# Optimization experiments

Hardware: AMD Instinct MI355X
Metric: run time of the kernel (lower is better)

Reference implementation:

```python
import jax, jax.numpy as jnp
import numpy as np
import math

D, H, FF = 1024, 16, 4096
B, L = 4, 1024

def setup_inputs() -> dict:
    key = jax.random.key(0)
    ks = jax.random.split(key, 20)
    g = lambda k, shp: jax.random.normal(k, shp, dtype=jnp.float32) * 0.02
    inp = {
        'x': jax.random.normal(ks[0], (B, L, D), dtype=jnp.float32),
        'encoder_output': jax.random.normal(ks[1], (B, L, D), dtype=jnp.float32),
        'src_mask': jnp.ones((1, 1, L, L), dtype=jnp.int32),
        'tgt_mask': jnp.tril(jnp.ones((L, L), dtype=jnp.int32))[None, None],
        'wq': g(ks[2], (D, D)), 'bq': jnp.zeros((D,), jnp.float32),
        'wk': g(ks[3], (D, D)), 'bk': jnp.zeros((D,), jnp.float32),
        'wv': g(ks[4], (D, D)), 'bv': jnp.zeros((D,), jnp.float32),
        'wo': g(ks[5], (D, D)), 'bo': jnp.zeros((D,), jnp.float32),
        'w1': g(ks[6], (FF, D)), 'b1': jnp.zeros((FF,), jnp.float32),
        'w2': g(ks[7], (D, FF)), 'b2': jnp.zeros((D,), jnp.float32),
        'g1': jnp.ones((D,), jnp.float32), 'be1': jnp.zeros((D,), jnp.float32),
        'g2': jnp.ones((D,), jnp.float32), 'be2': jnp.zeros((D,), jnp.float32),
    }
    return inp

def _layernorm(x, g, b, eps=1e-5):
    mu = jnp.mean(x, axis=-1, keepdims=True)
    var = jnp.var(x, axis=-1, keepdims=True)
    return (x - mu) * jax.lax.rsqrt(var + eps) * g + b

def _mha(q, k, v, mask, wq, bq, wk, bk, wv, bv, wo, bo):
    Bq, Lq, C = q.shape
    dh = C // H
    qh = (q @ wq.T + bq).reshape(Bq, Lq, H, dh)      # b q h d
    kh = (k @ wk.T + bk).reshape(Bq, -1, H, dh)       # b k h d
    vh = (v @ wv.T + bv).reshape(Bq, -1, H, dh)
    # NOTE: source scales by sqrt(C) (full model dim), not sqrt(head_dim)
    scores = jnp.einsum('bqhd,bkhd->bhqk', qh, kh) / math.sqrt(C)
    if mask is not None:
        scores = jnp.where(mask == 0, jnp.float32(-1e9), scores)
    attn = jax.nn.softmax(scores, axis=-1)
    out = jnp.einsum('bhqk,bkhd->bqhd', attn, vh).reshape(Bq, Lq, C)
    return out @ wo.T + bo

def reference(x, encoder_output, src_mask, tgt_mask,
              wq, bq, wk, bk, wv, bv, wo, bo,
              w1, b1, w2, b2, g1, be1, g2, be2):
    # self-attention (dropout identity in eval mode)
    y1 = _mha(x, x, x, tgt_mask, wq, bq, wk, bk, wv, bv, wo, bo)
    y1 = _layernorm(y1 + x, g1, be1)
    # cross-attention: source reuses attn1 weights and layer_norm1 (faithful)
    y2 = _mha(y1, encoder_output, encoder_output, src_mask, wq, bq, wk, bk, wv, bv, wo, bo)
    y2 = _layernorm(y1 + y2, g1, be1)
    # FFN + layer_norm2
    y = jax.nn.relu(y2 @ w1.T + b1) @ w2.T + b2
    return _layernorm(y2 + y, g2, be2)
```

## Files before the change

### kernel.cpp

```cpp
#include <hip/hip_runtime.h>
#include <hip/hip_bf16.h>

typedef __attribute__((ext_vector_type(8))) short short8;
typedef __attribute__((ext_vector_type(4))) float f32x4;
typedef __attribute__((ext_vector_type(4))) unsigned short ushort4v;

#define MFMA_BF16(a, b, c) __builtin_amdgcn_mfma_f32_16x16x32_bf16((a), (b), (c), 0, 0, 0)
#define AS1 __attribute__((address_space(1)))
#define AS3 __attribute__((address_space(3)))

__device__ __forceinline__ unsigned short f2b(float f) {
  unsigned u = __float_as_uint(f);
  u += 0x7fffu + ((u >> 16) & 1u);
  return (unsigned short)(u >> 16);
}

__device__ __forceinline__ size_t kpack_idx(int row, int col) {
  int b = row >> 10, l = row & 1023, h = col >> 6, d = col & 63;
  return ((size_t)(b * 16 + h) << 16) + l * 64 + (d ^ ((l & 7) << 3));
}

__global__ __launch_bounds__(256) void cast8(
    const float* s0, const float* s1, const float* s2, const float* s3,
    const float* s4, const float* s5, const float* s6, const float* s7,
    unsigned short* d0, unsigned short* d1, unsigned short* d2, unsigned short* d3,
    unsigned short* d4, unsigned short* d5, unsigned short* d6, unsigned short* d7,
    int n0, int n1, int n2, int n3, int n4, int n5, int n6, int n7) {
  const float* s; unsigned short* d; int n;
  switch (blockIdx.y) {
    case 0: s = s0; d = d0; n = n0; break;
    case 1: s = s1; d = d1; n = n1; break;
    case 2: s = s2; d = d2; n = n2; break;
    case 3: s = s3; d = d3; n = n3; break;
    case 4: s = s4; d = d4; n = n4; break;
    case 5: s = s5; d = d5; n = n5; break;
    case 6: s = s6; d = d6; n = n6; break;
    default: s = s7; d = d7; n = n7; break;
  }
  int stride = gridDim.x * blockDim.x;
  for (int i = blockIdx.x * blockDim.x + threadIdx.x; i < n; i += stride) {
    float4 v = reinterpret_cast<const float4*>(s)[i];
    ushort4v o;
    o.x = f2b(v.x); o.y = f2b(v.y); o.z = f2b(v.z); o.w = f2b(v.w);
    reinterpret_cast<ushort4v*>(d)[i] = o;
  }
}

template <int RELU, int RES, int OUTF, int OUTB, int TM>
__global__ __launch_bounds__(256) void gemm_bt(
    const unsigned short* __restrict__ A, const unsigned short* __restrict__ W,
    const float* __restrict__ bias, const float* __restrict__ resid,
    float* __restrict__ outF, unsigned short* __restrict__ outB,
    int M, int N, int K) {
  constexpr int MI = TM / 32;
  __shared__ unsigned short lA[TM * 64];
  __shared__ unsigned short lB[128 * 64];
  int nbn = N >> 7;
  int nwg = gridDim.x;
  int id = blockIdx.x;
  { int q = nwg >> 3; id = (id & 7) * q + (id >> 3); }
  int m0 = (id / nbn) * TM, n0 = (id % nbn) << 7;
  int lane = threadIdx.x & 63, wave = threadIdx.x >> 6;
  int wr = (wave >> 1) * (TM / 2), wc = (wave & 1) * 64;
  int rq = lane & 15, kq = (lane >> 4) * 8;
  int xr8 = (rq & 7) << 3;
  f32x4 acc[MI][4] = {};

  int t8 = threadIdx.x * 8;
  for (int kt = 0; kt < K; kt += 64) {
#pragma unroll
    for (int i = 0; i < MI; ++i) {
      int e = t8 + i * 2048;
      int row = e >> 6;
      int gcol = (((e >> 3) & 7) ^ (row & 7)) << 3;
      __builtin_amdgcn_global_load_lds(
          (const AS1 void*)(A + (size_t)(m0 + row) * K + kt + gcol),
          (AS3 void*)(lA + e), 16, 0, 0);
    }
#pragma unroll
    for (int i = 0; i < 4; ++i) {
      int e = t8 + i * 2048;
      int row = e >> 6;
      int gcol = (((e >> 3) & 7) ^ (row & 7)) << 3;
      __builtin_amdgcn_global_load_lds(
          (const AS1 void*)(W + (size_t)(n0 + row) * K + kt + gcol),
          (AS3 void*)(lB + e), 16, 0, 0);
    }
    __syncthreads();
#pragma unroll
    for (int s = 0; s < 2; ++s) {
      short8 af[MI], bf[4];
#pragma unroll
      for (int i = 0; i < MI; ++i)
        af[i] = *reinterpret_cast<const short8*>(lA + (wr + i * 16 + rq) * 64 + ((s * 32 + kq) ^ xr8));
#pragma unroll
      for (int j = 0; j < 4; ++j)
        bf[j] = *reinterpret_cast<const short8*>(lB + (wc + j * 16 + rq) * 64 + ((s * 32 + kq) ^ xr8));
#pragma unroll
      for (int i = 0; i < MI; ++i)
#pragma unroll
        for (int j = 0; j < 4; ++j)
          acc[i][j] = MFMA_BF16(af[i], bf[j], acc[i][j]);
    }
    __syncthreads();
  }

  int r0 = (lane >> 4) * 4;
#pragma unroll
  for (int i = 0; i < MI; ++i) {
#pragma unroll
    for (int j = 0; j < 4; ++j) {
      int row = m0 + wr + i * 16 + r0;
      int col = n0 + wc + j * 16 + rq;
      float bv = bias[col];
#pragma unroll
      for (int r = 0; r < 4; ++r) {
        float v = acc[i][j][r] + bv;
        if (RES) v += resid[(size_t)(row + r) * N + col];
        if (RELU) v = fmaxf(v, 0.0f);
        if (OUTF) outF[(size_t)(row + r) * N + col] = v;
        if (OUTB) outB[(size_t)(row + r) * N + col] = f2b(v);
      }
    }
  }
}

__global__ __launch_bounds__(256, 2) void gemm_qkv_f(
    const unsigned short* __restrict__ xb, const unsigned short* __restrict__ encb,
    const unsigned short* __restrict__ wq, const unsigned short* __restrict__ wk,
    const unsigned short* __restrict__ wv,
    const float* __restrict__ bq, const float* __restrict__ bk, const float* __restrict__ bv,
    unsigned short* __restrict__ qb, unsigned short* __restrict__ kp1,
    unsigned short* __restrict__ vp1, unsigned short* __restrict__ kp2,
    unsigned short* __restrict__ vp2) {
  __shared__ unsigned short lA[2][4096];
  __shared__ unsigned short lB[2][3][4096];
  int id = blockIdx.x;
  id = (id & 7) * 64 + (id >> 3);
  int sel = id >> 8;
  int idx = id & 255;
  int m0 = (idx >> 3) << 7, col0 = (idx & 7) << 7;
  int nW = sel ? 2 : 3;
  const unsigned short* A = sel ? encb : xb;
  const unsigned short* W0 = sel ? wk : wq;
  const unsigned short* W1 = sel ? wv : wk;
  const unsigned short* W2 = wv;
  int lane = threadIdx.x & 63, wave = threadIdx.x >> 6;
  int wr = (wave >> 1) * 64, wc = (wave & 1) * 64;
  int rq = lane & 15, kq = (lane >> 4) * 8;
  f32x4 acc[3][4][4] = {};

  int e0 = threadIdx.x * 8;
#define STG(KT, BUF)                                                            \
  {                                                                             \
    _Pragma("unroll") for (int i = 0; i < 2; ++i) {                             \
      int e = e0 + i * 2048;                                                    \
      int row = e >> 5, col = e & 31;                                           \
      __builtin_amdgcn_global_load_lds(                                         \
          (const AS1 void*)(A + (size_t)(m0 + row) * 1024 + (KT) + col),        \
          (AS3 void*)(&lA[BUF][e]), 16, 0, 0);                                  \
      __builtin_amdgcn_global_load_lds(                                         \
          (const AS1 void*)(W0 + (size_t)(col0 + row) * 1024 + (KT) + col),     \
          (AS3 void*)(&lB[BUF][0][e]), 16, 0, 0);                               \
      __builtin_amdgcn_global_load_lds(                                         \
          (const AS1 void*)(W1 + (size_t)(col0 + row) * 1024 + (KT) + col),     \
          (AS3 void*)(&lB[BUF][1][e]), 16, 0, 0);                               \
      if (!sel)                                                                 \
        __builtin_amdgcn_global_load_lds(                                       \
            (const AS1 void*)(W2 + (size_t)(col0 + row) * 1024 + (KT) + col),   \
            (AS3 void*)(&lB[BUF][2][e]), 16, 0, 0);                             \
    }                                                                           \
  }

  STG(0, 0);
  __syncthreads();
  for (int t = 0; t < 32; ++t) {
    int cur = t & 1;
    if (t + 1 < 32) STG((t + 1) << 5, cur ^ 1);
    short8 af[4];
#pragma unroll
    for (int i = 0; i < 4; ++i)
      af[i] = *reinterpret_cast<const short8*>(&lA[cur][(wr + i * 16 + rq) * 32 + kq]);
#pragma unroll
    for (int w = 0; w < 3; ++w) {
      if (w < nW) {
        short8 bf[4];
#pragma unroll
        for (int j = 0; j < 4; ++j)
          bf[j] = *reinterpret_cast<const short8*>(&lB[cur][w][(wc + j * 16 + rq) * 32 + kq]);
#pragma unroll
        for (int i = 0; i < 4; ++i)
#pragma unroll
          for (int j = 0; j < 4; ++j)
            acc[w][i][j] = MFMA_BF16(af[i], bf[j], acc[w][i][j]);
      }
    }
    __syncthreads();
  }
#undef STG

  int r0 = (lane >> 4) * 4;
#pragma unroll
  for (int w = 0; w < 3; ++w) {
    if (w >= nW) continue;
    const float* bias = sel ? (w == 0 ? bk : bv) : (w == 0 ? bq : (w == 1 ? bk : bv));
    unsigned short* outp = sel ? (w == 0 ? kp2 : vp2) : (w == 0 ? qb : (w == 1 ? kp1 : vp1));
    int pack = sel ? (w + 1) : w;
#pragma unroll
    for (int i = 0; i < 4; ++i) {
#pragma unroll
      for (int j = 0; j < 4; ++j) {
        int row0 = m0 + wr + i * 16 + r0;
        int col = col0 + wc + j * 16 + rq;
        float bv2 = bias[col];
        if (pack == 2) {
          int b = row0 >> 10, k0 = row0 & 1023, h = col >> 6, d = col & 63;
          size_t idx2 = ((size_t)((b * 16 + h) * 16 + (k0 >> 6)) << 12) + d * 64 + ((k0 & 63) ^ ((d & 7) << 3));
          ushort4v o;
          o.x = f2b(acc[w][i][j][0] + bv2);
          o.y = f2b(acc[w][i][j][1] + bv2);
          o.z = f2b(acc[w][i][j][2] + bv2);
          o.w = f2b(acc[w][i][j][3] + bv2);
          *reinterpret_cast<ushort4v*>(&outp[idx2]) = o;
        } else {
#pragma unroll
          for (int r = 0; r < 4; ++r) {
            int row = row0 + r;
            float v = acc[w][i][j][r] + bv2;
            if (pack == 0) outp[(size_t)row * 1024 + col] = f2b(v);
            else outp[kpack_idx(row, col)] = f2b(v);
          }
        }
      }
    }
  }
}

__device__ __forceinline__ void attn_step(
    const unsigned short* __restrict__ kcur, const unsigned short* __restrict__ vcur,
    unsigned short* __restrict__ plw, const short8* qf,
    f32x4* accd, float& m2, float& lsum,
    int rq, int hi, int kq, int xr, int wave, bool domask) {
  const float SC = 0.04508422f;
  f32x4 st[4];
  __builtin_amdgcn_s_setprio(1);
#pragma unroll
  for (int sub = 0; sub < 4; ++sub) {
    f32x4 z = {0.f, 0.f, 0.f, 0.f};
#pragma unroll
    for (int c = 0; c < 2; ++c) {
      short8 kf = *reinterpret_cast<const short8*>(
          &kcur[(sub * 16 + rq) * 64 + ((c * 32 + hi * 8) ^ xr)]);
      z = MFMA_BF16(kf, qf[c], z);
    }
    st[sub] = z * SC;
  }
  __builtin_amdgcn_s_setprio(0);
  if (domask) {
#pragma unroll
    for (int sub = 0; sub < 4; ++sub)
#pragma unroll
      for (int r = 0; r < 4; ++r)
        if (sub * 16 + hi * 4 + r > wave * 16 + rq) st[sub][r] = -1e9f;
  }
  f32x4 t0 = {fmaxf(st[0][0], st[1][0]), fmaxf(st[0][1], st[1][1]),
              fmaxf(st[0][2], st[1][2]), fmaxf(st[0][3], st[1][3])};
  f32x4 t1 = {fmaxf(st[2][0], st[3][0]), fmaxf(st[2][1], st[3][1]),
              fmaxf(st[2][2], st[3][2]), fmaxf(st[2][3], st[3][3])};
  float mx = fmaxf(fmaxf(fmaxf(t0[0], t1[0]), fmaxf(t0[1], t1[1])),
                   fmaxf(fmaxf(t0[2], t1[2]), fmaxf(t0[3], t1[3])));
  mx = fmaxf(mx, __shfl_xor(mx, 16, 64));
  mx = fmaxf(mx, __shfl_xor(mx, 32, 64));
  float mn = fmaxf(m2, mx);
  float al = exp2f(m2 - mn);
  m2 = mn;
  f32x4 e[4];
#pragma unroll
  for (int sub = 0; sub < 4; ++sub)
#pragma unroll
    for (int r = 0; r < 4; ++r) e[sub][r] = exp2f(st[sub][r] - mn);
  f32x4 s01 = e[0] + e[1], s23 = e[2] + e[3];
  f32x4 s = s01 + s23;
  float ps = (s[0] + s[1]) + (s[2] + s[3]);
  ps += __shfl_xor(ps, 16, 64);
  ps += __shfl_xor(ps, 32, 64);
  lsum = lsum * al + ps;
#pragma unroll
  for (int sub = 0; sub < 4; ++sub) {
    unsigned w0 = (unsigned)f2b(e[sub][0]) | ((unsigned)f2b(e[sub][1]) << 16);
    unsigned w1 = (unsigned)f2b(e[sub][2]) | ((unsigned)f2b(e[sub][3]) << 16);
    uint2 w = make_uint2(w0, w1);
    *reinterpret_cast<uint2*>(&plw[rq * 64 + ((sub * 16 + hi * 4) ^ xr)]) = w;
  }
  float alb[4];
#pragma unroll
  for (int r = 0; r < 4; ++r) alb[r] = __shfl(al, hi * 4 + r, 64);
#pragma unroll
  for (int d = 0; d < 4; ++d)
#pragma unroll
    for (int r = 0; r < 4; ++r) accd[d][r] *= alb[r];
  short8 pf[2];
#pragma unroll
  for (int c = 0; c < 2; ++c)
    pf[c] = *reinterpret_cast<const short8*>(&plw[rq * 64 + ((c * 32 + hi * 8) ^ xr)]);
  __builtin_amdgcn_s_setprio(1);
#pragma unroll
  for (int d = 0; d < 4; ++d) {
#pragma unroll
    for (int c = 0; c < 2; ++c) {
      short8 vf = *reinterpret_cast<const short8*>(
          &vcur[(d * 16 + rq) * 64 + ((c * 32 + hi * 8) ^ xr)]);
      accd[d] = MFMA_BF16(pf[c], vf, accd[d]);
    }
  }
  __builtin_amdgcn_s_setprio(0);
}

__global__ __launch_bounds__(256) void attn_kernel(
    const unsigned short* __restrict__ Q, const unsigned short* __restrict__ Kp,
    const unsigned short* __restrict__ Vp, unsigned short* __restrict__ O, int causal) {
  __shared__ unsigned short kls[2][4096];
  __shared__ unsigned short vls[2][4096];
  __shared__ unsigned short pls[4][1024];
  int id = blockIdx.x;
  int xcd = id & 7, j = id >> 3;
  int bh = xcd * 8 + (j & 7);
  int b = bh >> 4, h = bh & 15;
  int lane = threadIdx.x & 63, wave = threadIdx.x >> 6;
  int rq = lane & 15, hi = lane >> 4, kq = hi * 8;
  int xr = (rq & 7) << 3;
  int sb = wave * 1024 + lane * 8;
  const unsigned short* Kbh = Kp + ((size_t)bh << 16);
  const unsigned short* Vbh = Vp + ((size_t)bh << 16);
  unsigned short* plw = pls[wave];

  int p = j >> 3;
  int qtA = p;
  int qtB = causal ? (15 - p) : (p + 8);
  int lastA = causal ? qtA : 15;
  int nkt = causal ? (qtB + 1) : 16;

  int qrowA = qtA * 64 + wave * 16, qrowB = qtB * 64 + wave * 16;
  short8 qfA[2], qfB[2];
#pragma unroll
  for (int c = 0; c < 2; ++c) {
    qfA[c] = *reinterpret_cast<const short8*>(
        Q + (size_t)(b * 1024 + qrowA + rq) * 1024 + h * 64 + c * 32 + kq);
    qfB[c] = *reinterpret_cast<const short8*>(
        Q + (size_t)(b * 1024 + qrowB + rq) * 1024 + h * 64 + c * 32 + kq);
  }

  float mA = -1e30f, lsA = 0.f, mB = -1e30f, lsB = 0.f;
  f32x4 accA[4] = {}, accB[4] = {};

#pragma unroll
  for (int i = 0; i < 2; ++i) {
    __builtin_amdgcn_global_load_lds((const AS1 void*)(Kbh + sb + i * 512),
                                     (AS3 void*)(&kls[0][sb + i * 512]), 16, 0, 0);
    __builtin_amdgcn_global_load_lds((const AS1 void*)(Vbh + sb + i * 512),
                                     (AS3 void*)(&vls[0][sb + i * 512]), 16, 0, 0);
  }
  __syncthreads();

  int cur = 0;
  for (int kt = 0; kt < nkt; ++kt) {
    if (kt + 1 < nkt) {
      const unsigned short* kg = Kbh + (kt + 1) * 4096 + sb;
      const unsigned short* vg = Vbh + (kt + 1) * 4096 + sb;
#pragma unroll
      for (int i = 0; i < 2; ++i) {
        __builtin_amdgcn_global_load_lds((const AS1 void*)(kg + i * 512),
                                         (AS3 void*)(&kls[cur ^ 1][sb + i * 512]), 16, 0, 0);
        __builtin_amdgcn_global_load_lds((const AS1 void*)(vg + i * 512),
                                         (AS3 void*)(&vls[cur ^ 1][sb + i * 512]), 16, 0, 0);
      }
    }
    attn_step(kls[cur], vls[cur], plw, qfB, accB, mB, lsB, rq, hi, kq, xr, wave,
              causal && kt == qtB);
    if (kt <= lastA)
      attn_step(kls[cur], vls[cur], plw, qfA, accA, mA, lsA, rq, hi, kq, xr, wave,
                causal && kt == qtA);
    __syncthreads();
    cur ^= 1;
  }

  float lbA[4], lbB[4];
#pragma unroll
  for (int r = 0; r < 4; ++r) {
    lbA[r] = 1.0f / __shfl(lsA, hi * 4 + r, 64);
    lbB[r] = 1.0f / __shfl(lsB, hi * 4 + r, 64);
  }
#pragma unroll
  for (int d = 0; d < 4; ++d)
#pragma unroll
    for (int r = 0; r < 4; ++r) {
      O[(size_t)(b * 1024 + qrowA + hi * 4 + r) * 1024 + h * 64 + d * 16 + rq] =
          f2b(accA[d][r] * lbA[r]);
      O[(size_t)(b * 1024 + qrowB + hi * 4 + r) * 1024 + h * 64 + d * 16 + rq] =
          f2b(accB[d][r] * lbB[r]);
    }
}

template <int OUTF, int OUTB>
__global__ __launch_bounds__(256) void ln_kernel(const float* __restrict__ X,
                                                 const float* __restrict__ g,
                                                 const float* __restrict__ be,
                                                 float* __restrict__ outF,
                                                 unsigned short* __restrict__ outB) {
  __shared__ float red[2][4];
  int row = blockIdx.x;
  int t = threadIdx.x;
  const float* xr = X + (size_t)row * 1024;
  float4 v = reinterpret_cast<const float4*>(xr)[t];
  float s = v.x + v.y + v.z + v.w;
  float ss = v.x * v.x + v.y * v.y + v.z * v.z + v.w * v.w;
#pragma unroll
  for (int off = 1; off < 64; off <<= 1) {
    s += __shfl_xor(s, off, 64);
    ss += __shfl_xor(ss, off, 64);
  }
  int wave = t >> 6;
  if ((t & 63) == 0) { red[0][wave] = s; red[1][wave] = ss; }
  __syncthreads();
  s = red[0][0] + red[0][1] + red[0][2] + red[0][3];
  ss = red[1][0] + red[1][1] + red[1][2] + red[1][3];
  float mu = s * (1.f / 1024.f);
  float var = ss * (1.f / 1024.f) - mu * mu;
  float rs = rsqrtf(var + 1e-5f);
  float4 gv = reinterpret_cast<const float4*>(g)[t];
  float4 bv = reinterpret_cast<const float4*>(be)[t];
  float o0 = (v.x - mu) * rs * gv.x + bv.x;
  float o1 = (v.y - mu) * rs * gv.y + bv.y;
  float o2 = (v.z - mu) * rs * gv.z + bv.z;
  float o3 = (v.w - mu) * rs * gv.w + bv.w;
  if (OUTF) {
    float4 o = make_float4(o0, o1, o2, o3);
    reinterpret_cast<float4*>(outF + (size_t)row * 1024)[t] = o;
  }
  if (OUTB) {
    ushort4v o;
    o.x = f2b(o0); o.y = f2b(o1); o.z = f2b(o2); o.w = f2b(o3);
    reinterpret_cast<ushort4v*>(outB + (size_t)row * 1024)[t] = o;
  }
}

extern "C" void kernel_launch(void* const* d_in, const int* in_sizes, int n_in,
                              void* d_out, int out_size, void* d_ws, size_t ws_size,
                              hipStream_t stream) {
  const float* x   = (const float*)d_in[0];
  const float* enc = (const float*)d_in[1];
  const float* wq = (const float*)d_in[4];  const float* bq = (const float*)d_in[5];
  const float* wk = (const float*)d_in[6];  const float* bk = (const float*)d_in[7];
  const float* wv = (const float*)d_in[8];  const float* bv = (const float*)d_in[9];
  const float* wo = (const float*)d_in[10]; const float* bo = (const float*)d_in[11];
  const float* w1 = (const float*)d_in[12]; const float* b1 = (const float*)d_in[13];
  const float* w2 = (const float*)d_in[14]; const float* b2 = (const float*)d_in[15];
  const float* g1 = (const float*)d_in[16]; const float* be1 = (const float*)d_in[17];
  const float* g2 = (const float*)d_in[18]; const float* be2 = (const float*)d_in[19];
  float* out = (float*)d_out;

  const int M = 4096;
  char* ws = (char*)d_ws;
  size_t off = 0;
  auto alloc = [&](size_t bytes) -> char* {
    char* p = ws + off;
    off += (bytes + 255) & ~(size_t)255;
    return p;
  };
  unsigned short* xb   = (unsigned short*)alloc((size_t)M * 1024 * 2);
  unsigned short* encb = (unsigned short*)alloc((size_t)M * 1024 * 2);
  unsigned short* wqb  = (unsigned short*)alloc((size_t)1024 * 1024 * 2);
  unsigned short* wkb  = (unsigned short*)alloc((size_t)1024 * 1024 * 2);
  unsigned short* wvb  = (unsigned short*)alloc((size_t)1024 * 1024 * 2);
  unsigned short* wob  = (unsigned short*)alloc((size_t)1024 * 1024 * 2);
  unsigned short* w1b  = (unsigned short*)alloc((size_t)4096 * 1024 * 2);
  unsigned short* w2b  = (unsigned short*)alloc((size_t)4096 * 1024 * 2);
  unsigned short* qb   = (unsigned short*)alloc((size_t)M * 1024 * 2);
  unsigned short* kp1  = (unsigned short*)alloc((size_t)M * 1024 * 2);
  unsigned short* vp1  = (unsigned short*)alloc((size_t)M * 1024 * 2);
  unsigned short* kp2  = (unsigned short*)alloc((size_t)M * 1024 * 2);
  unsigned short* vp2  = (unsigned short*)alloc((size_t)M * 1024 * 2);
  unsigned short* ab   = (unsigned short*)alloc((size_t)M * 1024 * 2);
  float* s1 = (float*)alloc((size_t)M * 1024 * 4);
  float* y1 = (float*)alloc((size_t)M * 1024 * 4);
  unsigned short* hb = kp1;
  unsigned short* y1b = xb;
  unsigned short* y2b = qb;
  float* y2 = y1;

  dim3 b256(256);
  cast8<<<dim3(256, 8), b256, 0, stream>>>(
      x, enc, wq, wk, wv, wo, w1, w2,
      xb, encb, wqb, wkb, wvb, wob, w1b, w2b,
      M * 1024 / 4, M * 1024 / 4, 262144, 262144, 262144, 262144,
      4096 * 1024 / 4, 4096 * 1024 / 4);

  gemm_qkv_f<<<512, b256, 0, stream>>>(xb, encb, wqb, wkb, wvb, bq, bk, bv,
                                       qb, kp1, vp1, kp2, vp2);

  attn_kernel<<<512, b256, 0, stream>>>(qb, kp1, vp1, ab, 1);
  gemm_bt<0, 1, 1, 0, 64><<<512, b256, 0, stream>>>(ab, wob, bo, x, s1, nullptr, M, 1024, 1024);
  ln_kernel<1, 1><<<4096, b256, 0, stream>>>(s1, g1, be1, y1, y1b);

  gemm_bt<0, 0, 0, 1, 64><<<512, b256, 0, stream>>>(y1b, wqb, bq, nullptr, nullptr, qb, M, 1024, 1024);
  attn_kernel<<<512, b256, 0, stream>>>(qb, kp2, vp2, ab, 0);
  gemm_bt<0, 1, 1, 0, 64><<<512, b256, 0, stream>>>(ab, wob, bo, y1, s1, nullptr, M, 1024, 1024);
  ln_kernel<1, 1><<<4096, b256, 0, stream>>>(s1, g1, be1, y2, y2b);

  gemm_bt<1, 0, 0, 1, 128><<<1024, b256, 0, stream>>>(y2b, w1b, b1, nullptr, nullptr, hb, M, 4096, 1024);
  gemm_bt<0, 1, 1, 0, 64><<<512, b256, 0, stream>>>(hb, w2b, b2, y2, s1, nullptr, M, 1024, 4096);
  ln_kernel<1, 0><<<4096, b256, 0, stream>>>(s1, g2, be2, out, nullptr);

  (void)in_sizes; (void)n_in; (void)out_size; (void)ws_size;
}
```

Baseline: 341.5 us.

## Swizzle QKV GEMM LDS, add lazy softmax rescale, one q-tile per attention block

The QKV GEMM now XOR-swizzles the 16-byte column chunks it loads into LDS, and its fragment reads use the matching swizzle, to avoid LDS bank conflicts. The attention softmax skips rescaling the accumulator and running sum when no row's max grows by more than a threshold (a lazy-rescale trick), which saves exp and multiply work. The attention kernel also stops pairing two query tiles per block and launches twice as many blocks, one q-tile each, with causal tiles ordered heaviest first. The trade-off is less K/V reuse per block and more total K/V loads, in exchange for simpler blocks and better load balance.

```diff
diff --git a/kernel.cpp b/kernel.cpp
--- a/kernel.cpp
+++ b/kernel.cpp
@@ -148,6 +148,7 @@
   int lane = threadIdx.x & 63, wave = threadIdx.x >> 6;
   int wr = (wave >> 1) * 64, wc = (wave & 1) * 64;
   int rq = lane & 15, kq = (lane >> 4) * 8;
+  int xk = ((rq >> 1) & 3) << 3;
   f32x4 acc[3][4][4] = {};
 
   int e0 = threadIdx.x * 8;
@@ -155,19 +156,20 @@
   {                                                                             \
     _Pragma("unroll") for (int i = 0; i < 2; ++i) {                             \
       int e = e0 + i * 2048;                                                    \
-      int row = e >> 5, col = e & 31;                                           \
+      int row = e >> 5;                                                         \
+      int gcol = ((((e >> 3) & 3) ^ ((row >> 1) & 3)) << 3);                    \
       __builtin_amdgcn_global_load_lds(                                         \
-          (const AS1 void*)(A + (size_t)(m0 + row) * 1024 + (KT) + col),        \
+          (const AS1 void*)(A + (size_t)(m0 + row) * 1024 + (KT) + gcol),       \
           (AS3 void*)(&lA[BUF][e]), 16, 0, 0);                                  \
       __builtin_amdgcn_global_load_lds(                                         \
-          (const AS1 void*)(W0 + (size_t)(col0 + row) * 1024 + (KT) + col),     \
+          (const AS1 void*)(W0 + (size_t)(col0 + row) * 1024 + (KT) + gcol),    \
           (AS3 void*)(&lB[BUF][0][e]), 16, 0, 0);                               \
       __builtin_amdgcn_global_load_lds(                                         \
-          (const AS1 void*)(W1 + (size_t)(col0 + row) * 1024 + (KT) + col),     \
+          (const AS1 void*)(W1 + (size_t)(col0 + row) * 1024 + (KT) + gcol),    \
           (AS3 void*)(&lB[BUF][1][e]), 16, 0, 0);                               \
       if (!sel)                                                                 \
         __builtin_amdgcn_global_load_lds(                                       \
-            (const AS1 void*)(W2 + (size_t)(col0 + row) * 1024 + (KT) + col),   \
+            (const AS1 void*)(W2 + (size_t)(col0 + row) * 1024 + (KT) + gcol),  \
             (AS3 void*)(&lB[BUF][2][e]), 16, 0, 0);                             \
     }                                                                           \
   }
@@ -180,14 +182,14 @@
     short8 af[4];
 #pragma unroll
     for (int i = 0; i < 4; ++i)
-      af[i] = *reinterpret_cast<const short8*>(&lA[cur][(wr + i * 16 + rq) * 32 + kq]);
+      af[i] = *reinterpret_cast<const short8*>(&lA[cur][(wr + i * 16 + rq) * 32 + (kq ^ xk)]);
 #pragma unroll
     for (int w = 0; w < 3; ++w) {
       if (w < nW) {
         short8 bf[4];
 #pragma unroll
         for (int j = 0; j < 4; ++j)
-          bf[j] = *reinterpret_cast<const short8*>(&lB[cur][w][(wc + j * 16 + rq) * 32 + kq]);
+          bf[j] = *reinterpret_cast<const short8*>(&lB[cur][w][(wc + j * 16 + rq) * 32 + (kq ^ xk)]);
 #pragma unroll
         for (int i = 0; i < 4; ++i)
 #pragma unroll
@@ -271,9 +273,13 @@
                    fmaxf(fmaxf(t0[2], t1[2]), fmaxf(t0[3], t1[3])));
   mx = fmaxf(mx, __shfl_xor(mx, 16, 64));
   mx = fmaxf(mx, __shfl_xor(mx, 32, 64));
-  float mn = fmaxf(m2, mx);
-  float al = exp2f(m2 - mn);
-  m2 = mn;
+  int skip = __all(mx <= m2 + 4.0f);
+  float mn = m2, al = 1.0f;
+  if (!skip) {
+    mn = fmaxf(m2, mx);
+    al = exp2f(m2 - mn);
+    m2 = mn;
+  }
   f32x4 e[4];
 #pragma unroll
   for (int sub = 0; sub < 4; ++sub)
@@ -284,7 +290,6 @@
   float ps = (s[0] + s[1]) + (s[2] + s[3]);
   ps += __shfl_xor(ps, 16, 64);
   ps += __shfl_xor(ps, 32, 64);
-  lsum = lsum * al + ps;
 #pragma unroll
   for (int sub = 0; sub < 4; ++sub) {
     unsigned w0 = (unsigned)f2b(e[sub][0]) | ((unsigned)f2b(e[sub][1]) << 16);
@@ -292,13 +297,18 @@
     uint2 w = make_uint2(w0, w1);
     *reinterpret_cast<uint2*>(&plw[rq * 64 + ((sub * 16 + hi * 4) ^ xr)]) = w;
   }
-  float alb[4];
-#pragma unroll
-  for (int r = 0; r < 4; ++r) alb[r] = __shfl(al, hi * 4 + r, 64);
-#pragma unroll
-  for (int d = 0; d < 4; ++d)
-#pragma unroll
-    for (int r = 0; r < 4; ++r) accd[d][r] *= alb[r];
+  if (skip) {
+    lsum += ps;
+  } else {
+    lsum = lsum * al + ps;
+    float alb[4];
+#pragma unroll
+    for (int r = 0; r < 4; ++r) alb[r] = __shfl(al, hi * 4 + r, 64);
+#pragma unroll
+    for (int d = 0; d < 4; ++d)
+#pragma unroll
+      for (int r = 0; r < 4; ++r) accd[d][r] *= alb[r];
+  }
   short8 pf[2];
 #pragma unroll
   for (int c = 0; c < 2; ++c)
@@ -323,9 +333,11 @@
   __shared__ unsigned short vls[2][4096];
   __shared__ unsigned short pls[4][1024];
   int id = blockIdx.x;
-  int xcd = id & 7, j = id >> 3;
-  int bh = xcd * 8 + (j & 7);
+  int xcd = id & 7, rest = id >> 3;
+  int qtsel = rest & 15, bhi = rest >> 4;
+  int bh = xcd * 8 + bhi;
   int b = bh >> 4, h = bh & 15;
+  int qt = causal ? (15 - qtsel) : qtsel;
   int lane = threadIdx.x & 63, wave = threadIdx.x >> 6;
   int rq = lane & 15, hi = lane >> 4, kq = hi * 8;
   int xr = (rq & 7) << 3;
@@ -334,24 +346,16 @@
   const unsigned short* Vbh = Vp + ((size_t)bh << 16);
   unsigned short* plw = pls[wave];
 
-  int p = j >> 3;
-  int qtA = p;
-  int qtB = causal ? (15 - p) : (p + 8);
-  int lastA = causal ? qtA : 15;
-  int nkt = causal ? (qtB + 1) : 16;
-
-  int qrowA = qtA * 64 + wave * 16, qrowB = qtB * 64 + wave * 16;
-  short8 qfA[2], qfB[2];
-#pragma unroll
-  for (int c = 0; c < 2; ++c) {
-    qfA[c] = *reinterpret_cast<const short8*>(
-        Q + (size_t)(b * 1024 + qrowA + rq) * 1024 + h * 64 + c * 32 + kq);
-    qfB[c] = *reinterpret_cast<const short8*>(
-        Q + (size_t)(b * 1024 + qrowB + rq) * 1024 + h * 64 + c * 32 + kq);
-  }
-
-  float mA = -1e30f, lsA = 0.f, mB = -1e30f, lsB = 0.f;
-  f32x4 accA[4] = {}, accB[4] = {};
+  int nkt = causal ? (qt + 1) : 16;
+  int qrow0 = qt * 64 + wave * 16;
+  short8 qf[2];
+#pragma unroll
+  for (int c = 0; c < 2; ++c)
+    qf[c] = *reinterpret_cast<const short8*>(
+        Q + (size_t)(b * 1024 + qrow0 + rq) * 1024 + h * 64 + c * 32 + kq);
+
+  float m2 = -1e30f, lsum = 0.f;
+  f32x4 accd[4] = {};
 
 #pragma unroll
   for (int i = 0; i < 2; ++i) {
@@ -375,30 +379,21 @@
                                          (AS3 void*)(&vls[cur ^ 1][sb + i * 512]), 16, 0, 0);
       }
     }
-    attn_step(kls[cur], vls[cur], plw, qfB, accB, mB, lsB, rq, hi, kq, xr, wave,
-              causal && kt == qtB);
-    if (kt <= lastA)
-      attn_step(kls[cur], vls[cur], plw, qfA, accA, mA, lsA, rq, hi, kq, xr, wave,
-                causal && kt == qtA);
+    attn_step(kls[cur], vls[cur], plw, qf, accd, m2, lsum, rq, hi, kq, xr, wave,
+              causal && kt == qt);
     __syncthreads();
     cur ^= 1;
   }
 
-  float lbA[4], lbB[4];
-#pragma unroll
-  for (int r = 0; r < 4; ++r) {
-    lbA[r] = 1.0f / __shfl(lsA, hi * 4 + r, 64);
-    lbB[r] = 1.0f / __shfl(lsB, hi * 4 + r, 64);
-  }
+  float lb[4];
+#pragma unroll
+  for (int r = 0; r < 4; ++r) lb[r] = 1.0f / __shfl(lsum, hi * 4 + r, 64);
 #pragma unroll
   for (int d = 0; d < 4; ++d)
 #pragma unroll
-    for (int r = 0; r < 4; ++r) {
-      O[(size_t)(b * 1024 + qrowA + hi * 4 + r) * 1024 + h * 64 + d * 16 + rq] =
-          f2b(accA[d][r] * lbA[r]);
-      O[(size_t)(b * 1024 + qrowB + hi * 4 + r) * 1024 + h * 64 + d * 16 + rq] =
-          f2b(accB[d][r] * lbB[r]);
-    }
+    for (int r = 0; r < 4; ++r)
+      O[(size_t)(b * 1024 + qrow0 + hi * 4 + r) * 1024 + h * 64 + d * 16 + rq] =
+          f2b(accd[d][r] * lb[r]);
 }
 
 template <int OUTF, int OUTB>
@@ -498,12 +493,12 @@
   gemm_qkv_f<<<512, b256, 0, stream>>>(xb, encb, wqb, wkb, wvb, bq, bk, bv,
                                        qb, kp1, vp1, kp2, vp2);
 
-  attn_kernel<<<512, b256, 0, stream>>>(qb, kp1, vp1, ab, 1);
+  attn_kernel<<<1024, b256, 0, stream>>>(qb, kp1, vp1, ab, 1);
   gemm_bt<0, 1, 1, 0, 64><<<512, b256, 0, stream>>>(ab, wob, bo, x, s1, nullptr, M, 1024, 1024);
   ln_kernel<1, 1><<<4096, b256, 0, stream>>>(s1, g1, be1, y1, y1b);
 
   gemm_bt<0, 0, 0, 1, 64><<<512, b256, 0, stream>>>(y1b, wqb, bq, nullptr, nullptr, qb, M, 1024, 1024);
-  attn_kernel<<<512, b256, 0, stream>>>(qb, kp2, vp2, ab, 0);
+  attn_kernel<<<1024, b256, 0, stream>>>(qb, kp2, vp2, ab, 0);
   gemm_bt<0, 1, 1, 0, 64><<<512, b256, 0, stream>>>(ab, wob, bo, y1, s1, nullptr, M, 1024, 1024);
   ln_kernel<1, 1><<<4096, b256, 0, stream>>>(s1, g1, be1, y2, y2b);
 
```

Result: no change. 346.3 us (+1.4%).
